# Kernel optimization log

Measured on AMD Instinct MI355X. Metric: run time of the kernel, lower is better.

## Reference

```python
import jax, jax.numpy as jnp
import numpy as np

B, T, E, H, DL, CC, K = 64, 2048, 512, 128, 1024, 32, 31


def setup_inputs() -> dict:
    key = jax.random.key(0)
    ks = jax.random.split(key, 8)
    return {
        "encoder_output": jax.random.normal(ks[0], (B, T, E), jnp.float32),
        "processed_encoder_output": jax.random.normal(ks[1], (B, T, H), jnp.float32),
        "lstm_output": jax.random.normal(ks[2], (B, 1, DL), jnp.float32),
        "attention_weights_cum": jax.random.uniform(ks[3], (B, T), jnp.float32),
        # learned params (torch Linear stores [out, in]; y = x @ W.T)
        "W_lstm": jax.random.normal(ks[4], (H, DL), jnp.float32) * 0.02,
        "conv_w": jax.random.normal(ks[5], (CC, 1, K), jnp.float32) * 0.1,
        "W_loc": jax.random.normal(ks[6], (H, CC), jnp.float32) * 0.1,
        "W_e": jax.random.normal(ks[7], (1, H), jnp.float32) * 0.1,
    }


def _forward(encoder_output, processed_encoder_output, lstm_output,
             attention_weights_cum, W_lstm, conv_w, W_loc, W_e):
    # [B,1,1024] @ [1024,128] -> [B,1,128]
    processed_lstm = jnp.einsum('bqd,hd->bqh', lstm_output, W_lstm)
    # location conv: [B,1,T] -> [B,32,T], same padding
    loc = lax.conv_general_dilated(
        attention_weights_cum[:, None, :], conv_w,
        window_strides=(1,), padding=[(K // 2, K // 2)],
        dimension_numbers=('NCH', 'OIH', 'NCH'))
    # transpose to [B,T,32] then dense to [B,T,128]
    processed_attn = jnp.einsum('bct,hc->bth', loc, W_loc)
    # additive energies: [B,T,128] -> [B,T]
    energies = jnp.einsum('bth,oh->bto',
                          jnp.tanh(processed_lstm + processed_attn + processed_encoder_output),
                          W_e)[..., 0]
    attention_weights = jax.nn.softmax(energies, axis=1)  # [B,T]
    # bmm: [B,1,T] @ [B,T,E] -> [B,1,E]
    attention_context = jnp.einsum('bt,bte->be', attention_weights, encoder_output)[:, None, :]
    return attention_context, attention_weights

from jax import lax


def reference(encoder_output, processed_encoder_output, lstm_output,
              attention_weights_cum, W_lstm, conv_w, W_loc, W_e):
    return _forward(encoder_output, processed_encoder_output, lstm_output,
                    attention_weights_cum, W_lstm, conv_w, W_loc, W_e)
```

## Files before the change

kernel.cpp:

```cpp
#include <hip/hip_runtime.h>
#include <math.h>


#define BB 64
#define TT 2048
#define EE 512
#define HH 128
#define DLL 1024
#define CCC 32
#define KK 31

#define WS_FW   0
#define WS_PL   4096
#define WS_EN   12288
#define WS_ST   143360
#define WS_PART 144384

__global__ __launch_bounds__(256) void k0_prep(const float* __restrict__ lstm,
                                               const float* __restrict__ Wl,
                                               const float* __restrict__ cw,
                                               const float* __restrict__ Wloc,
                                               float* __restrict__ ws) {
  const int blk = blockIdx.x;
  const int tid = threadIdx.x;
  if (blk < 2048) {
    const int wave = tid >> 6, lane = tid & 63;
    const int wg = blk * 4 + wave;
    const int b = wg >> 7, h = wg & 127;
    const float4* wr = (const float4*)(Wl + (size_t)h * DLL);
    const float4* lr = (const float4*)(lstm + (size_t)b * DLL);
    float s = 0.f;
#pragma unroll
    for (int m = 0; m < 4; ++m) {
      float4 a = wr[m * 64 + lane];
      float4 c = lr[m * 64 + lane];
      s += a.x * c.x + a.y * c.y + a.z * c.z + a.w * c.w;
    }
#pragma unroll
    for (int m = 1; m < 64; m <<= 1) s += __shfl_xor(s, m, 64);
    if (lane == 0) ws[WS_PL + b * HH + h] = s;
  } else {
    __shared__ __align__(16) float wl_s[HH * CCC];
    __shared__ __align__(16) float cw_s[CCC * KK];
#pragma unroll
    for (int m = 0; m < 4; ++m)
      ((float4*)wl_s)[tid + 256 * m] = ((const float4*)Wloc)[tid + 256 * m];
    if (tid < 248) ((float4*)cw_s)[tid] = ((const float4*)cw)[tid];
    __syncthreads();
    const int h = tid >> 1;
    const int kbase = (tid & 1) * 16;
    const int kn = (tid & 1) ? 15 : 16;
    for (int kk = 0; kk < kn; ++kk) {
      const int k = kbase + kk;
      float s = 0.f;
#pragma unroll
      for (int c = 0; c < CCC; ++c) s += wl_s[h * CCC + c] * cw_s[c * KK + k];
      ws[WS_FW + h * 32 + k] = s;
    }
    if (tid & 1) ws[WS_FW + h * 32 + 31] = 0.f;
  }
}

__global__ __launch_bounds__(512, 4) void k1_fused(const float* __restrict__ pe,
                                                   const float* __restrict__ aw,
                                                   const float* __restrict__ We,
                                                   const float* __restrict__ enc,
                                                   float* __restrict__ ws) {
  const int b = blockIdx.y;
  const int chunk = blockIdx.x;
  const int t0 = chunk * 256;
  const int tid = threadIdx.x;
  const int wave = tid >> 6, lane = tid & 63;

  __shared__ __align__(16) float fw_s[HH * 32];
  __shared__ __align__(16) float aw_s[288];
  __shared__ float pl_s[128];
  __shared__ float we_s[128];
  __shared__ __align__(16) float pp[4][4][64];
  __shared__ float w_s[256];
  __shared__ __align__(16) float4 acc_s[128];
  __shared__ float m_arr[4], s_arr[4];
  __shared__ int flag_s[4], cnt_s[4];

  {
    const float4* src = (const float4*)(ws + WS_FW);
    float4* dst = (float4*)fw_s;
    dst[tid] = src[tid];
    dst[tid + 512] = src[tid + 512];
  }
  if (tid < 288) {
    const int tg = t0 - 16 + tid;
    aw_s[tid] = (tg >= 0 && tg < TT) ? aw[b * TT + tg] : 0.f;
  }
  if (tid < 128) {
    pl_s[tid] = ws[WS_PL + b * HH + tid];
    we_s[tid] = We[tid];
  }
  if (tid < 4) { flag_s[tid] = 0; cnt_s[tid] = 0; }
  __syncthreads();

  if (wave < 4) {
    const int hbase = wave * 32;
#pragma unroll 1
    for (int sub = 0; sub < 4; ++sub) {
      const int lt = sub * 64 + lane;
      float wreg[32];
#pragma unroll
      for (int k = 0; k < 32; ++k) wreg[k] = aw_s[lt + 1 + k];
      const float4* pr4 = (const float4*)(pe + ((size_t)b * TT + t0 + lt) * HH) +
                          (hbase >> 2);
      float4 ptv[8];
#pragma unroll
      for (int i = 0; i < 8; ++i) ptv[i] = pr4[i];
      float pts[32];
#pragma unroll
      for (int i = 0; i < 8; ++i) {
        pts[4 * i + 0] = ptv[i].x; pts[4 * i + 1] = ptv[i].y;
        pts[4 * i + 2] = ptv[i].z; pts[4 * i + 3] = ptv[i].w;
      }
      float partial = 0.f;
#pragma unroll 2
      for (int hh = 0; hh < 32; ++hh) {
        const int h = hbase + hh;
        const float4* fr = (const float4*)&fw_s[h * 32];
        float a0 = pl_s[h] + pts[hh];
        float a1 = 0.f;
#pragma unroll
        for (int q = 0; q < 8; ++q) {
          const float4 f = fr[q];
          a0 = fmaf(f.x, wreg[4 * q + 0], a0);
          a1 = fmaf(f.y, wreg[4 * q + 1], a1);
          a0 = fmaf(f.z, wreg[4 * q + 2], a0);
          a1 = fmaf(f.w, wreg[4 * q + 3], a1);
        }
        const float x = a0 + a1;
        const float th = 1.f - 2.f / (__expf(2.f * x) + 1.f);
        partial = fmaf(we_s[h], th, partial);
      }
      pp[sub][wave][lane] = partial;

      int old = 0;
      if (lane == 0)
        old = __hip_atomic_fetch_add(&cnt_s[sub], 1, __ATOMIC_ACQ_REL,
                                     __HIP_MEMORY_SCOPE_WORKGROUP);
      old = __shfl(old, 0, 64);
      if (old == 3) {
        const float e = pp[sub][0][lane] + pp[sub][1][lane] +
                        pp[sub][2][lane] + pp[sub][3][lane];
        ws[WS_EN + b * TT + t0 + lt] = e;
        float m = e;
#pragma unroll
        for (int s = 1; s < 64; s <<= 1) m = fmaxf(m, __shfl_xor(m, s, 64));
        float p = __expf(e - m);
#pragma unroll
        for (int s = 1; s < 64; s <<= 1) p += __shfl_xor(p, s, 64);
        w_s[lt] = __expf(e - m);
        if (lane == 0) { m_arr[sub] = m; s_arr[sub] = p; }
        __hip_atomic_store(&flag_s[sub], 1, __ATOMIC_RELEASE,
                           __HIP_MEMORY_SCOPE_WORKGROUP);
      }
    }
    __syncthreads();
  } else {
    const int cid = tid - 256;
    const int c4 = cid & 127;
    const int tp = cid >> 7;
    const float4* enc4 = (const float4*)(enc + ((size_t)b * TT + t0) * EE);
    float4 a0 = {0.f, 0.f, 0.f, 0.f}, a1 = {0.f, 0.f, 0.f, 0.f};
    float mrun = -3.4e38f;
#pragma unroll 1
    for (int sub = 0; sub < 4; ++sub) {
      while (!__hip_atomic_load(&flag_s[sub], __ATOMIC_ACQUIRE,
                                __HIP_MEMORY_SCOPE_WORKGROUP))
        __builtin_amdgcn_s_sleep(2);
      const float mi = m_arr[sub];
      const float mnew = fmaxf(mrun, mi);
      const float so = __expf(mrun - mnew);
      const float sc = __expf(mi - mnew);
      a0.x *= so; a0.y *= so; a0.z *= so; a0.w *= so;
      a1.x *= so; a1.y *= so; a1.z *= so; a1.w *= so;
      const float* wp = &w_s[sub * 64];
#pragma unroll 8
      for (int i = 0; i < 32; ++i) {
        const int t = 2 * i + tp;
        const float w = wp[t] * sc;
        const float4 v = enc4[(size_t)(sub * 64 + t) * 128 + c4];
        if (i & 1) {
          a1.x = fmaf(w, v.x, a1.x); a1.y = fmaf(w, v.y, a1.y);
          a1.z = fmaf(w, v.z, a1.z); a1.w = fmaf(w, v.w, a1.w);
        } else {
          a0.x = fmaf(w, v.x, a0.x); a0.y = fmaf(w, v.y, a0.y);
          a0.z = fmaf(w, v.z, a0.z); a0.w = fmaf(w, v.w, a0.w);
        }
      }
      mrun = mnew;
    }
    a0.x += a1.x; a0.y += a1.y; a0.z += a1.z; a0.w += a1.w;
    if (tp == 1) acc_s[c4] = a0;
    __syncthreads();
    if (tp == 0) {
      const float4 o = acc_s[c4];
      a0.x += o.x; a0.y += o.y; a0.z += o.z; a0.w += o.w;
      ((float4*)(ws + WS_PART))[(size_t)(b * 8 + chunk) * 128 + c4] = a0;
    }
    if (cid == 0) {
      const float mb = fmaxf(fmaxf(m_arr[0], m_arr[1]),
                             fmaxf(m_arr[2], m_arr[3]));
      float sb = 0.f;
#pragma unroll
      for (int c = 0; c < 4; ++c) sb += s_arr[c] * __expf(m_arr[c] - mb);
      float* st = ws + WS_ST + (b * 8 + chunk) * 2;
      st[0] = mb;
      st[1] = sb;
    }
  }
}

__global__ __launch_bounds__(256) void k2_combine(const float* __restrict__ ws,
                                                  float* __restrict__ wts,
                                                  float* __restrict__ ctx) {
  const int b = blockIdx.x;
  const int tid = threadIdx.x;

  const float* st = ws + WS_ST + b * 16;
  float mb = -3.4e38f;
#pragma unroll
  for (int c = 0; c < 8; ++c) mb = fmaxf(mb, st[2 * c]);
  float S = 0.f;
#pragma unroll
  for (int c = 0; c < 8; ++c) S += st[2 * c + 1] * __expf(st[2 * c] - mb);
  const float inv = 1.f / S;

  __shared__ float esc[8];
  if (tid < 8) esc[tid] = __expf(st[2 * tid] - mb) * inv;
  __syncthreads();

  const float4* en4 = (const float4*)(ws + WS_EN + (size_t)b * TT);
  float4* w4 = (float4*)(wts + (size_t)b * TT);
#pragma unroll
  for (int j = 0; j < 2; ++j) {
    const float4 e = en4[tid * 2 + j];
    float4 w;
    w.x = __expf(e.x - mb) * inv;
    w.y = __expf(e.y - mb) * inv;
    w.z = __expf(e.z - mb) * inv;
    w.w = __expf(e.w - mb) * inv;
    w4[tid * 2 + j] = w;
  }

  const float2* p2 = (const float2*)(ws + WS_PART) + (size_t)b * 8 * 256 + tid;
  float2 s = {0.f, 0.f};
#pragma unroll
  for (int c = 0; c < 8; ++c) {
    const float2 v = p2[c * 256];
    s.x = fmaf(esc[c], v.x, s.x);
    s.y = fmaf(esc[c], v.y, s.y);
  }
  ((float2*)ctx)[b * 256 + tid] = s;
}

extern "C" void kernel_launch(void* const* d_in, const int* in_sizes, int n_in,
                              void* d_out, int out_size, void* d_ws, size_t ws_size,
                              hipStream_t stream) {
  const float* enc  = (const float*)d_in[0];
  const float* pe   = (const float*)d_in[1];
  const float* lstm = (const float*)d_in[2];
  const float* awc  = (const float*)d_in[3];
  const float* Wl   = (const float*)d_in[4];
  const float* cw   = (const float*)d_in[5];
  const float* Wloc = (const float*)d_in[6];
  const float* We   = (const float*)d_in[7];

  float* out = (float*)d_out;
  float* ctx = out;
  float* wts = out + BB * EE;
  float* ws = (float*)d_ws;

  k0_prep<<<2049, 256, 0, stream>>>(lstm, Wl, cw, Wloc, ws);
  k1_fused<<<dim3(8, BB), 512, 0, stream>>>(pe, awc, We, enc, ws);
  k2_combine<<<BB, 256, 0, stream>>>(ws, wts, ctx);
}
```

Baseline: 78.29 us.

## Split energy sub-chunks to 32 timesteps for finer producer-consumer overlap

The energy-computing waves now handle 32 timesteps per sub-step, with each half-wave covering 16 hidden units, across 8 sub-steps instead of 4. The context-accumulating waves can therefore start on encoder rows sooner and the pipeline fill latency shrinks. In exchange there are more flag handshakes and rescale steps, and half the lanes sit idle during the reductions. The combine kernel is also spread over 4x64 blocks, computing the chunk scale factors per thread instead of through shared memory.

```diff
diff --git a/kernel.cpp b/kernel.cpp
--- a/kernel.cpp
+++ b/kernel.cpp
@@ -76,11 +76,11 @@
   __shared__ __align__(16) float aw_s[288];
   __shared__ float pl_s[128];
   __shared__ float we_s[128];
-  __shared__ __align__(16) float pp[4][4][64];
+  __shared__ __align__(16) float pp[8][4][64];
   __shared__ float w_s[256];
   __shared__ __align__(16) float4 acc_s[128];
-  __shared__ float m_arr[4], s_arr[4];
-  __shared__ int flag_s[4], cnt_s[4];
+  __shared__ float m_arr[8], s_arr[8];
+  __shared__ int flag_s[8], cnt_s[8];
 
   {
     const float4* src = (const float4*)(ws + WS_FW);
@@ -96,32 +96,34 @@
     pl_s[tid] = ws[WS_PL + b * HH + tid];
     we_s[tid] = We[tid];
   }
-  if (tid < 4) { flag_s[tid] = 0; cnt_s[tid] = 0; }
+  if (tid < 8) { flag_s[tid] = 0; cnt_s[tid] = 0; }
   __syncthreads();
 
   if (wave < 4) {
-    const int hbase = wave * 32;
+    const int th = lane >> 5;
+    const int lt32 = lane & 31;
+    const int hb = wave * 32 + th * 16;
 #pragma unroll 1
-    for (int sub = 0; sub < 4; ++sub) {
-      const int lt = sub * 64 + lane;
+    for (int sub = 0; sub < 8; ++sub) {
+      const int lt = sub * 32 + lt32;
       float wreg[32];
 #pragma unroll
       for (int k = 0; k < 32; ++k) wreg[k] = aw_s[lt + 1 + k];
-      const float4* pr4 = (const float4*)(pe + ((size_t)b * TT + t0 + lt) * HH) +
-                          (hbase >> 2);
-      float4 ptv[8];
-#pragma unroll
-      for (int i = 0; i < 8; ++i) ptv[i] = pr4[i];
-      float pts[32];
-#pragma unroll
-      for (int i = 0; i < 8; ++i) {
+      const float4* pr4 =
+          (const float4*)(pe + ((size_t)b * TT + t0 + lt) * HH) + (hb >> 2);
+      float4 ptv[4];
+#pragma unroll
+      for (int i = 0; i < 4; ++i) ptv[i] = pr4[i];
+      float pts[16];
+#pragma unroll
+      for (int i = 0; i < 4; ++i) {
         pts[4 * i + 0] = ptv[i].x; pts[4 * i + 1] = ptv[i].y;
         pts[4 * i + 2] = ptv[i].z; pts[4 * i + 3] = ptv[i].w;
       }
       float partial = 0.f;
 #pragma unroll 2
-      for (int hh = 0; hh < 32; ++hh) {
-        const int h = hbase + hh;
+      for (int hh = 0; hh < 16; ++hh) {
+        const int h = hb + hh;
         const float4* fr = (const float4*)&fw_s[h * 32];
         float a0 = pl_s[h] + pts[hh];
         float a1 = 0.f;
@@ -134,8 +136,8 @@
           a1 = fmaf(f.w, wreg[4 * q + 3], a1);
         }
         const float x = a0 + a1;
-        const float th = 1.f - 2.f / (__expf(2.f * x) + 1.f);
-        partial = fmaf(we_s[h], th, partial);
+        const float thv = 1.f - 2.f / (__expf(2.f * x) + 1.f);
+        partial = fmaf(we_s[h], thv, partial);
       }
       pp[sub][wave][lane] = partial;
 
@@ -145,16 +147,20 @@
                                      __HIP_MEMORY_SCOPE_WORKGROUP);
       old = __shfl(old, 0, 64);
       if (old == 3) {
-        const float e = pp[sub][0][lane] + pp[sub][1][lane] +
-                        pp[sub][2][lane] + pp[sub][3][lane];
-        ws[WS_EN + b * TT + t0 + lt] = e;
+        const int lt2 = lane & 31;
+        float e = 0.f;
+#pragma unroll
+        for (int w2 = 0; w2 < 4; ++w2)
+          e += pp[sub][w2][lt2] + pp[sub][w2][lt2 + 32];
+        if (lane < 32) ws[WS_EN + b * TT + t0 + sub * 32 + lane] = e;
         float m = e;
 #pragma unroll
         for (int s = 1; s < 64; s <<= 1) m = fmaxf(m, __shfl_xor(m, s, 64));
-        float p = __expf(e - m);
+        const float ex = __expf(e - m);
+        float p = (lane < 32) ? ex : 0.f;
 #pragma unroll
         for (int s = 1; s < 64; s <<= 1) p += __shfl_xor(p, s, 64);
-        w_s[lt] = __expf(e - m);
+        if (lane < 32) w_s[sub * 32 + lane] = ex;
         if (lane == 0) { m_arr[sub] = m; s_arr[sub] = p; }
         __hip_atomic_store(&flag_s[sub], 1, __ATOMIC_RELEASE,
                            __HIP_MEMORY_SCOPE_WORKGROUP);
@@ -169,7 +175,7 @@
     float4 a0 = {0.f, 0.f, 0.f, 0.f}, a1 = {0.f, 0.f, 0.f, 0.f};
     float mrun = -3.4e38f;
 #pragma unroll 1
-    for (int sub = 0; sub < 4; ++sub) {
+    for (int sub = 0; sub < 8; ++sub) {
       while (!__hip_atomic_load(&flag_s[sub], __ATOMIC_ACQUIRE,
                                 __HIP_MEMORY_SCOPE_WORKGROUP))
         __builtin_amdgcn_s_sleep(2);
@@ -179,12 +185,12 @@
       const float sc = __expf(mi - mnew);
       a0.x *= so; a0.y *= so; a0.z *= so; a0.w *= so;
       a1.x *= so; a1.y *= so; a1.z *= so; a1.w *= so;
-      const float* wp = &w_s[sub * 64];
+      const float* wp = &w_s[sub * 32];
 #pragma unroll 8
-      for (int i = 0; i < 32; ++i) {
+      for (int i = 0; i < 16; ++i) {
         const int t = 2 * i + tp;
         const float w = wp[t] * sc;
-        const float4 v = enc4[(size_t)(sub * 64 + t) * 128 + c4];
+        const float4 v = enc4[(size_t)(sub * 32 + t) * 128 + c4];
         if (i & 1) {
           a1.x = fmaf(w, v.x, a1.x); a1.y = fmaf(w, v.y, a1.y);
           a1.z = fmaf(w, v.z, a1.z); a1.w = fmaf(w, v.w, a1.w);
@@ -204,11 +210,12 @@
       ((float4*)(ws + WS_PART))[(size_t)(b * 8 + chunk) * 128 + c4] = a0;
     }
     if (cid == 0) {
-      const float mb = fmaxf(fmaxf(m_arr[0], m_arr[1]),
-                             fmaxf(m_arr[2], m_arr[3]));
+      float mb = -3.4e38f;
+#pragma unroll
+      for (int c = 0; c < 8; ++c) mb = fmaxf(mb, m_arr[c]);
       float sb = 0.f;
 #pragma unroll
-      for (int c = 0; c < 4; ++c) sb += s_arr[c] * __expf(m_arr[c] - mb);
+      for (int c = 0; c < 8; ++c) sb += s_arr[c] * __expf(m_arr[c] - mb);
       float* st = ws + WS_ST + (b * 8 + chunk) * 2;
       st[0] = mb;
       st[1] = sb;
@@ -219,7 +226,8 @@
 __global__ __launch_bounds__(256) void k2_combine(const float* __restrict__ ws,
                                                   float* __restrict__ wts,
                                                   float* __restrict__ ctx) {
-  const int b = blockIdx.x;
+  const int q = blockIdx.x;
+  const int b = blockIdx.y;
   const int tid = threadIdx.x;
 
   const float* st = ws + WS_ST + b * 16;
@@ -231,32 +239,33 @@
   for (int c = 0; c < 8; ++c) S += st[2 * c + 1] * __expf(st[2 * c] - mb);
   const float inv = 1.f / S;
 
-  __shared__ float esc[8];
-  if (tid < 8) esc[tid] = __expf(st[2 * tid] - mb) * inv;
-  __syncthreads();
-
-  const float4* en4 = (const float4*)(ws + WS_EN + (size_t)b * TT);
-  float4* w4 = (float4*)(wts + (size_t)b * TT);
-#pragma unroll
-  for (int j = 0; j < 2; ++j) {
-    const float4 e = en4[tid * 2 + j];
-    float4 w;
-    w.x = __expf(e.x - mb) * inv;
-    w.y = __expf(e.y - mb) * inv;
-    w.z = __expf(e.z - mb) * inv;
-    w.w = __expf(e.w - mb) * inv;
-    w4[tid * 2 + j] = w;
-  }
-
-  const float2* p2 = (const float2*)(ws + WS_PART) + (size_t)b * 8 * 256 + tid;
-  float2 s = {0.f, 0.f};
-#pragma unroll
-  for (int c = 0; c < 8; ++c) {
-    const float2 v = p2[c * 256];
-    s.x = fmaf(esc[c], v.x, s.x);
-    s.y = fmaf(esc[c], v.y, s.y);
-  }
-  ((float2*)ctx)[b * 256 + tid] = s;
+  {
+    const float4* en4 = (const float4*)(ws + WS_EN + (size_t)b * TT) + q * 128;
+    float4* w4 = (float4*)(wts + (size_t)b * TT) + q * 128;
+    if (tid < 128) {
+      const float4 e = en4[tid];
+      float4 w;
+      w.x = __expf(e.x - mb) * inv;
+      w.y = __expf(e.y - mb) * inv;
+      w.z = __expf(e.z - mb) * inv;
+      w.w = __expf(e.w - mb) * inv;
+      w4[tid] = w;
+    }
+  }
+
+  if (tid < 64) {
+    const int col = q * 64 + tid;
+    const float2* p2 = (const float2*)(ws + WS_PART) + (size_t)b * 8 * 256 + col;
+    float2 s = {0.f, 0.f};
+#pragma unroll
+    for (int c = 0; c < 8; ++c) {
+      const float2 v = p2[c * 256];
+      const float es = __expf(st[2 * c] - mb) * inv;
+      s.x = fmaf(es, v.x, s.x);
+      s.y = fmaf(es, v.y, s.y);
+    }
+    ((float2*)ctx)[b * 256 + col] = s;
+  }
 }
 
 extern "C" void kernel_launch(void* const* d_in, const int* in_sizes, int n_in,
@@ -278,5 +287,5 @@
 
   k0_prep<<<2049, 256, 0, stream>>>(lstm, Wl, cw, Wloc, ws);
   k1_fused<<<dim3(8, BB), 512, 0, stream>>>(pe, awc, We, enc, ws);
-  k2_combine<<<BB, 256, 0, stream>>>(ws, wts, ctx);
-}
+  k2_combine<<<dim3(4, BB), 256, 0, stream>>>(ws, wts, ctx);
+}
```

Measured after the change: 75.99 us. 2.9% less time.
